# Kernel tuning notes

Hardware: AMD Instinct MI355X
Metric: run time of the kernel (lower is better)

## Reference

```python
import jax, jax.numpy as jnp
import numpy as np

B, NQ, NK = 4, 384, 384
D_EQUI, D_QINV, D_KVINV = 64, 256, 256
D_MSG, D_FF, D_OUT = 64, 128, 64
IN_FEATS = 2 * D_MSG + D_EQUI  # 192


def setup_inputs() -> dict:
    key = jax.random.key(0)
    ks = jax.random.split(key, 12)
    s = lambda k, shp, fan: jax.random.normal(k, shp, jnp.float32) / np.sqrt(fan)
    return {
        "q_equi": jax.random.normal(ks[0], (B, NQ, 3, D_EQUI), jnp.float32),
        "q_inv": jax.random.normal(ks[1], (B, NQ, D_QINV), jnp.float32),
        "k_equi": jax.random.normal(ks[2], (B, NK, 3, D_EQUI), jnp.float32),
        "k_inv": jax.random.normal(ks[3], (B, NK, D_KVINV), jnp.float32),
        "Wq": s(ks[4], (D_QINV, D_MSG), D_QINV),
        "bq": jnp.zeros((D_MSG,), jnp.float32),
        "Wk": s(ks[5], (D_KVINV, D_MSG), D_KVINV),
        "bk": jnp.zeros((D_MSG,), jnp.float32),
        "W1": s(ks[6], (IN_FEATS, D_FF), IN_FEATS),
        "b1": jnp.zeros((D_FF,), jnp.float32),
        "W2": s(ks[7], (D_FF, D_OUT), D_FF),
        "b2": jnp.zeros((D_OUT,), jnp.float32),
    }


def reference(q_equi, q_inv, k_equi, k_inv, Wq, bq, Wk, bk, W1, b1, W2, b2):
    # dotprods over the 3 spatial coords, per equi-channel: [B, Nq, Nk, d_equi]
    dotprods = jnp.einsum("bqcd,bkcd->bqkd", q_equi, k_equi)
    q_msg = q_inv @ Wq + bq  # [B, Nq, d_msg]
    k_msg = k_inv @ Wk + bk  # [B, Nk, d_msg]
    b, nq, dm = q_msg.shape
    nk = k_msg.shape[1]
    # expand + concat -> [B, Nq, Nk, in_feats]
    feats = jnp.concatenate(
        [
            jnp.broadcast_to(q_msg[:, :, None, :], (b, nq, nk, dm)),
            jnp.broadcast_to(k_msg[:, None, :, :], (b, nq, nk, dm)),
            dotprods,
        ],
        axis=-1,
    )
    h = jax.nn.silu(feats @ W1 + b1)  # [B, Nq, Nk, d_ff]
    return h @ W2 + b2  # [B, Nq, Nk, d_out]
```

## Files before the change

kernel.cpp:

```cpp
#include <hip/hip_runtime.h>
#include <stdint.h>
#include <stddef.h>

#define NQ 384
#define NK 384

typedef __attribute__((ext_vector_type(4))) float float4_;
typedef __attribute__((ext_vector_type(8))) short short8;

__device__ __forceinline__ short f2bf(float f) {
  union { float f; uint32_t u; } v; v.f = f;
  uint32_t u = v.u;
  uint32_t r = (u + 0x7fffu + ((u >> 16) & 1u)) >> 16;
  return (short)r;
}

__global__ __launch_bounds__(128) void prep_kernel(
    const float* __restrict__ q_inv, const float* __restrict__ k_inv,
    const float* __restrict__ Wq, const float* __restrict__ bq,
    const float* __restrict__ Wk, const float* __restrict__ bk,
    const float* __restrict__ W1, const float* __restrict__ b1,
    const float* __restrict__ W2,
    float* __restrict__ A1, float* __restrict__ A2,
    short* __restrict__ W1dfrag, short* __restrict__ W2frag)
{
  int bid = blockIdx.x;
  int t = threadIdx.x;

  if (bid == 3072) {
    for (int idx = t; idx < 8192; idx += 128) {
      int fi = idx >> 9;
      int l  = (idx >> 3) & 63;
      int i  = idx & 7;
      {
        int n = fi >> 1, s = fi & 1;
        int d = s * 32 + ((l >> 4) << 3) + i;
        int f = n * 16 + (l & 15);
        W1dfrag[idx] = f2bf(W1[(128 + d) * 128 + f]);
      }
      {
        int n2 = fi >> 2, s2 = fi & 3;
        int k = s2 * 32 + ((l >> 4) << 3) + i;
        int o = n2 * 16 + (l & 15);
        W2frag[idx] = f2bf(W2[k * 64 + o]);
      }
    }
    return;
  }

  int half = bid / 1536;
  int idx = bid - half * 1536;
  const float* inv  = (half ? k_inv : q_inv) + (size_t)idx * 256;
  const float* W    = half ? Wk : Wq;
  const float* bias = half ? bk : bq;

  __shared__ float sinv[256];
  __shared__ float part[2][64];
  __shared__ float smsg[64];

  sinv[t] = inv[t];
  sinv[t + 128] = inv[t + 128];
  __syncthreads();

  {
    int f = t & 63, hh = t >> 6;
    float acc = 0.f;
    const float* wp = W + hh * 128 * 64 + f;
    const float* ip = sinv + hh * 128;
    #pragma unroll 4
    for (int j = 0; j < 128; ++j) acc += ip[j] * wp[j * 64];
    part[hh][f] = acc;
  }
  __syncthreads();
  if (t < 64) smsg[t] = part[0][t] + part[1][t] + bias[t];
  __syncthreads();

  {
    int n = t;
    const float* w1p = W1 + (half ? 64 : 0) * 128 + n;
    float acc = half ? 0.f : b1[n];
    #pragma unroll 8
    for (int f = 0; f < 64; ++f) acc += smsg[f] * w1p[f * 128];
    (half ? A2 : A1)[(size_t)idx * 128 + n] = acc;
  }
}

__global__ __launch_bounds__(512) void main_kernel(
    const float* __restrict__ q_equi, const float* __restrict__ k_equi,
    const float* __restrict__ A1, const float* __restrict__ A2,
    const short* __restrict__ W1dfrag, const short* __restrict__ W2frag,
    const float* __restrict__ b2, float* __restrict__ out)
{
  int bid = blockIdx.x;
  int b = bid / 576;
  int rem = bid - b * 576;
  int tq = rem / 24, tk = rem - (rem / 24) * 24;
  int q0 = tq * 16, k0 = tk * 16;

  __shared__ __align__(16) char smem[65536];
  float* sQ = (float*)smem;
  float* sK = (float*)(smem + 13056);

  int tid = threadIdx.x;
  int w = tid >> 6, l = tid & 63;
  int g = l >> 4, r16 = l & 15;

  const float* qsrc = q_equi + ((size_t)(b * NQ + q0)) * 192;
  const float* ksrc = k_equi + ((size_t)(b * NK + k0)) * 192;
  for (int j = tid; j < 3072; j += 512) {
    int rr = j / 192, cd = j - rr * 192;
    int c = cd >> 6, d = cd & 63;
    int li = c * 1088 + rr * 68 + d;
    sQ[li] = qsrc[j];
    sK[li] = ksrc[j];
  }
  __syncthreads();

  short8 afrag[2][2];
  #pragma unroll
  for (int s = 0; s < 2; ++s) {
    int d0 = s * 32 + g * 8;
    float4_ kva[3], kvb[3];
    #pragma unroll
    for (int c = 0; c < 3; ++c) {
      kva[c] = *(const float4_*)&sK[c * 1088 + r16 * 68 + d0];
      kvb[c] = *(const float4_*)&sK[c * 1088 + r16 * 68 + d0 + 4];
    }
    #pragma unroll
    for (int m = 0; m < 2; ++m) {
      int qi = 2 * w + m;
      float4_ qva[3], qvb[3];
      #pragma unroll
      for (int c = 0; c < 3; ++c) {
        qva[c] = *(const float4_*)&sQ[c * 1088 + qi * 68 + d0];
        qvb[c] = *(const float4_*)&sQ[c * 1088 + qi * 68 + d0 + 4];
      }
      short8 af;
      #pragma unroll
      for (int i = 0; i < 4; ++i) {
        float da = qva[0][i] * kva[0][i] + qva[1][i] * kva[1][i] + qva[2][i] * kva[2][i];
        float db = qvb[0][i] * kvb[0][i] + qvb[1][i] * kvb[1][i] + qvb[2][i] * kvb[2][i];
        af[i]     = f2bf(da);
        af[i + 4] = f2bf(db);
      }
      afrag[m][s] = af;
    }
  }

  float4_ acc1[2][8];
  const float* A1p = A1 + ((size_t)(b * NQ + q0)) * 128;
  const float* A2p = A2 + ((size_t)(b * NK + k0)) * 128;
  #pragma unroll
  for (int n = 0; n < 8; ++n) {
    int f = n * 16 + r16;
    float a2v0 = A2p[(g * 4 + 0) * 128 + f];
    float a2v1 = A2p[(g * 4 + 1) * 128 + f];
    float a2v2 = A2p[(g * 4 + 2) * 128 + f];
    float a2v3 = A2p[(g * 4 + 3) * 128 + f];
    #pragma unroll
    for (int m = 0; m < 2; ++m) {
      float a1v = A1p[(2 * w + m) * 128 + f];
      acc1[m][n] = (float4_){a1v + a2v0, a1v + a2v1, a1v + a2v2, a1v + a2v3};
    }
  }
  #pragma unroll
  for (int n = 0; n < 8; ++n) {
    #pragma unroll
    for (int s = 0; s < 2; ++s) {
      short8 bf = *(const short8*)&W1dfrag[(((n * 2 + s) * 64) + l) * 8];
      #pragma unroll
      for (int m = 0; m < 2; ++m)
        acc1[m][n] = __builtin_amdgcn_mfma_f32_16x16x32_bf16(afrag[m][s], bf, acc1[m][n], 0, 0, 0);
    }
  }
  __syncthreads();

  #pragma unroll
  for (int m = 0; m < 2; ++m) {
    int pbase = (2 * w + m) * 16 + g * 4;
    #pragma unroll
    for (int n = 0; n < 8; ++n) {
      int col = n * 16 + r16;
      #pragma unroll
      for (int rr = 0; rr < 4; ++rr) {
        float x = acc1[m][n][rr];
        float sig = 1.f / (1.f + __expf(-x));
        int p = pbase + rr;
        int byte = (p * 256 + col * 2) ^ ((p & 7) << 4);
        *(short*)(smem + byte) = f2bf(x * sig);
      }
    }
  }
  __syncthreads();

  short8 w2f[4][4];
  #pragma unroll
  for (int n2 = 0; n2 < 4; ++n2)
    #pragma unroll
    for (int s2 = 0; s2 < 4; ++s2)
      w2f[n2][s2] = *(const short8*)&W2frag[(((n2 * 4 + s2) * 64) + l) * 8];

  float4_ acc2[2][4];
  #pragma unroll
  for (int m = 0; m < 2; ++m)
    #pragma unroll
    for (int n2 = 0; n2 < 4; ++n2)
      acc2[m][n2] = (float4_){0.f, 0.f, 0.f, 0.f};

  #pragma unroll
  for (int m = 0; m < 2; ++m) {
    int row = (2 * w + m) * 16 + r16;
    #pragma unroll
    for (int s2 = 0; s2 < 4; ++s2) {
      int byte = (row * 256 + (s2 * 32 + g * 8) * 2) ^ ((row & 7) << 4);
      short8 ha = *(const short8*)(smem + byte);
      #pragma unroll
      for (int n2 = 0; n2 < 4; ++n2)
        acc2[m][n2] = __builtin_amdgcn_mfma_f32_16x16x32_bf16(ha, w2f[n2][s2], acc2[m][n2], 0, 0, 0);
    }
  }

  float* outp = out + ((size_t)(b * NQ + q0) * NK + k0) * 64;
  #pragma unroll
  for (int n2 = 0; n2 < 4; ++n2) {
    float b2v = b2[n2 * 16 + r16];
    #pragma unroll
    for (int m = 0; m < 2; ++m) {
      int qi = 2 * w + m;
      #pragma unroll
      for (int rr = 0; rr < 4; ++rr) {
        int ki = g * 4 + rr;
        outp[((size_t)qi * NK + ki) * 64 + n2 * 16 + r16] = acc2[m][n2][rr] + b2v;
      }
    }
  }
}

extern "C" void kernel_launch(void* const* d_in, const int* in_sizes, int n_in,
                              void* d_out, int out_size, void* d_ws, size_t ws_size,
                              hipStream_t stream) {
  (void)in_sizes; (void)n_in; (void)out_size; (void)ws_size;
  const float* q_equi = (const float*)d_in[0];
  const float* q_inv  = (const float*)d_in[1];
  const float* k_equi = (const float*)d_in[2];
  const float* k_inv  = (const float*)d_in[3];
  const float* Wq = (const float*)d_in[4];
  const float* bq = (const float*)d_in[5];
  const float* Wk = (const float*)d_in[6];
  const float* bk = (const float*)d_in[7];
  const float* W1 = (const float*)d_in[8];
  const float* b1 = (const float*)d_in[9];
  const float* W2 = (const float*)d_in[10];
  const float* b2 = (const float*)d_in[11];
  float* out = (float*)d_out;

  char* ws = (char*)d_ws;
  float* A1      = (float*)(ws);
  float* A2      = (float*)(ws + 786432);
  short* W1dfrag = (short*)(ws + 1572864);
  short* W2frag  = (short*)(ws + 1589248);

  prep_kernel<<<3073, 128, 0, stream>>>(q_inv, k_inv, Wq, bq, Wk, bk, W1, b1, W2,
                                        A1, A2, W1dfrag, W2frag);
  main_kernel<<<2304, 512, 0, stream>>>(q_equi, k_equi, A1, A2, W1dfrag, W2frag, b2, out);
}
```

Measured before the change: 253.2 us.

## Fold projection weights into W1, transpose MFMA operands, process q rows per-wave

The prep stage now precomputes Wq·W1a and Wk·W1b plus bias constants in a small kernel, then projects q_inv/k_inv directly to 128-wide A1/A2 with 8 rows per block instead of one row per block. The main kernel swaps MFMA operand order so accumulators hold consecutive output features, allowing float4 loads of A1/A2 and float4 stores of the output. It processes each of the two q rows per wave sequentially through a per-wave LDS tile, halving shared memory and dropping a block barrier. This adds a third kernel launch and changes the fp32 association of the projection sums.

After: 295.3 us. 1.17x slower.

```diff
diff --git a/kernel.cpp b/kernel.cpp
--- a/kernel.cpp
+++ b/kernel.cpp
@@ -1,4 +1,5 @@
 #include <hip/hip_runtime.h>
+#include <hip/hip_bf16.h>
 #include <stdint.h>
 #include <stddef.h>
 
@@ -7,6 +8,7 @@
 
 typedef __attribute__((ext_vector_type(4))) float float4_;
 typedef __attribute__((ext_vector_type(8))) short short8;
+typedef __attribute__((ext_vector_type(2))) unsigned int uint2_;
 
 __device__ __forceinline__ short f2bf(float f) {
   union { float f; uint32_t u; } v; v.f = f;
@@ -15,74 +17,94 @@
   return (short)r;
 }
 
-__global__ __launch_bounds__(128) void prep_kernel(
-    const float* __restrict__ q_inv, const float* __restrict__ k_inv,
-    const float* __restrict__ Wq, const float* __restrict__ bq,
-    const float* __restrict__ Wk, const float* __restrict__ bk,
+__device__ __forceinline__ unsigned int pk2(float lo, float hi) {
+  __hip_bfloat162 r = __float22bfloat162_rn(make_float2(lo, hi));
+  union { __hip_bfloat162 b; unsigned int u; } u; u.b = r;
+  return u.u;
+}
+
+__global__ __launch_bounds__(256) void prep0(
+    const float* __restrict__ Wq, const float* __restrict__ Wk,
     const float* __restrict__ W1, const float* __restrict__ b1,
+    const float* __restrict__ bq, const float* __restrict__ bk,
     const float* __restrict__ W2,
-    float* __restrict__ A1, float* __restrict__ A2,
+    float* __restrict__ Wqc, float* __restrict__ Wkc,
+    float* __restrict__ c1, float* __restrict__ c2,
     short* __restrict__ W1dfrag, short* __restrict__ W2frag)
 {
-  int bid = blockIdx.x;
-  int t = threadIdx.x;
-
-  if (bid == 3072) {
-    for (int idx = t; idx < 8192; idx += 128) {
+  int bid = blockIdx.x, t = threadIdx.x;
+  if (bid < 32) {
+    int side = bid >> 4;
+    int r0 = (bid & 15) * 16;
+    const float* W = side ? Wk : Wq;
+    const float* W1s = W1 + side * 64 * 128;
+    float* Wc = side ? Wkc : Wqc;
+    __shared__ float sW[16][64];
+    for (int j = t; j < 1024; j += 256) sW[j >> 6][j & 63] = W[(r0 + (j >> 6)) * 64 + (j & 63)];
+    __syncthreads();
+    int c = t & 127, rg = (t >> 7) * 8;
+    float acc[8] = {0.f, 0.f, 0.f, 0.f, 0.f, 0.f, 0.f, 0.f};
+    for (int k = 0; k < 64; ++k) {
+      float wv = W1s[k * 128 + c];
+      #pragma unroll
+      for (int j = 0; j < 8; ++j) acc[j] += sW[rg + j][k] * wv;
+    }
+    for (int j = 0; j < 8; ++j) Wc[(r0 + rg + j) * 128 + c] = acc[j];
+  } else if (bid == 32) {
+    if (t < 256) {
+      int c = t & 127, side = t >> 7;
+      const float* bias = side ? bk : bq;
+      const float* W1s = W1 + side * 64 * 128;
+      float acc = side ? 0.f : b1[c];
+      for (int k = 0; k < 64; ++k) acc += bias[k] * W1s[k * 128 + c];
+      (side ? c2 : c1)[c] = acc;
+    }
+  } else {
+    for (int idx = t; idx < 8192; idx += 256) {
       int fi = idx >> 9;
       int l  = (idx >> 3) & 63;
       int i  = idx & 7;
-      {
-        int n = fi >> 1, s = fi & 1;
+      { int n = fi >> 1, s = fi & 1;
         int d = s * 32 + ((l >> 4) << 3) + i;
         int f = n * 16 + (l & 15);
-        W1dfrag[idx] = f2bf(W1[(128 + d) * 128 + f]);
-      }
-      {
-        int n2 = fi >> 2, s2 = fi & 3;
+        W1dfrag[idx] = f2bf(W1[(128 + d) * 128 + f]); }
+      { int n2 = fi >> 2, s2 = fi & 3;
         int k = s2 * 32 + ((l >> 4) << 3) + i;
         int o = n2 * 16 + (l & 15);
-        W2frag[idx] = f2bf(W2[k * 64 + o]);
-      }
-    }
-    return;
-  }
-
-  int half = bid / 1536;
-  int idx = bid - half * 1536;
-  const float* inv  = (half ? k_inv : q_inv) + (size_t)idx * 256;
-  const float* W    = half ? Wk : Wq;
-  const float* bias = half ? bk : bq;
-
-  __shared__ float sinv[256];
-  __shared__ float part[2][64];
-  __shared__ float smsg[64];
-
-  sinv[t] = inv[t];
-  sinv[t + 128] = inv[t + 128];
+        W2frag[idx] = f2bf(W2[k * 64 + o]); }
+    }
+  }
+}
+
+__global__ __launch_bounds__(256) void prep1(
+    const float* __restrict__ q_inv, const float* __restrict__ k_inv,
+    const float* __restrict__ Wqc, const float* __restrict__ Wkc,
+    const float* __restrict__ c1, const float* __restrict__ c2,
+    float* __restrict__ A1, float* __restrict__ A2)
+{
+  int bid = blockIdx.x, t = threadIdx.x;
+  int row0 = bid * 8;
+  int side = row0 >= 1536;
+  int r0 = row0 - side * 1536;
+  const float* inv = (side ? k_inv : q_inv) + (size_t)r0 * 256;
+  const float* Wc  = side ? Wkc : Wqc;
+  const float* cc  = side ? c2 : c1;
+  float* A = (side ? A2 : A1) + (size_t)r0 * 128;
+
+  __shared__ float sI[8][256];
+  for (int j = t; j < 2048; j += 256) sI[j >> 8][j & 255] = inv[j];
   __syncthreads();
 
-  {
-    int f = t & 63, hh = t >> 6;
-    float acc = 0.f;
-    const float* wp = W + hh * 128 * 64 + f;
-    const float* ip = sinv + hh * 128;
-    #pragma unroll 4
-    for (int j = 0; j < 128; ++j) acc += ip[j] * wp[j * 64];
-    part[hh][f] = acc;
-  }
-  __syncthreads();
-  if (t < 64) smsg[t] = part[0][t] + part[1][t] + bias[t];
-  __syncthreads();
-
-  {
-    int n = t;
-    const float* w1p = W1 + (half ? 64 : 0) * 128 + n;
-    float acc = half ? 0.f : b1[n];
-    #pragma unroll 8
-    for (int f = 0; f < 64; ++f) acc += smsg[f] * w1p[f * 128];
-    (half ? A2 : A1)[(size_t)idx * 128 + n] = acc;
-  }
+  int c = t & 127, rg = (t >> 7) * 4;
+  float acc[4] = {0.f, 0.f, 0.f, 0.f};
+  for (int k = 0; k < 256; ++k) {
+    float wv = Wc[k * 128 + c];
+    #pragma unroll
+    for (int j = 0; j < 4; ++j) acc[j] += sI[rg + j][k] * wv;
+  }
+  float cv = cc[c];
+  #pragma unroll
+  for (int j = 0; j < 4; ++j) A[(size_t)(rg + j) * 128 + c] = acc[j] + cv;
 }
 
 __global__ __launch_bounds__(512) void main_kernel(
@@ -97,7 +119,7 @@
   int tq = rem / 24, tk = rem - (rem / 24) * 24;
   int q0 = tq * 16, k0 = tk * 16;
 
-  __shared__ __align__(16) char smem[65536];
+  __shared__ __align__(16) char smem[32768];
   float* sQ = (float*)smem;
   float* sK = (float*)(smem + 13056);
 
@@ -135,103 +157,85 @@
         qva[c] = *(const float4_*)&sQ[c * 1088 + qi * 68 + d0];
         qvb[c] = *(const float4_*)&sQ[c * 1088 + qi * 68 + d0 + 4];
       }
-      short8 af;
+      float da[4], db[4];
       #pragma unroll
       for (int i = 0; i < 4; ++i) {
-        float da = qva[0][i] * kva[0][i] + qva[1][i] * kva[1][i] + qva[2][i] * kva[2][i];
-        float db = qvb[0][i] * kvb[0][i] + qvb[1][i] * kvb[1][i] + qvb[2][i] * kvb[2][i];
-        af[i]     = f2bf(da);
-        af[i + 4] = f2bf(db);
-      }
-      afrag[m][s] = af;
-    }
-  }
-
-  float4_ acc1[2][8];
+        da[i] = qva[0][i] * kva[0][i] + qva[1][i] * kva[1][i] + qva[2][i] * kva[2][i];
+        db[i] = qvb[0][i] * kvb[0][i] + qvb[1][i] * kvb[1][i] + qvb[2][i] * kvb[2][i];
+      }
+      union { short8 s8; unsigned int u[4]; } au;
+      au.u[0] = pk2(da[0], da[1]);
+      au.u[1] = pk2(da[2], da[3]);
+      au.u[2] = pk2(db[0], db[1]);
+      au.u[3] = pk2(db[2], db[3]);
+      afrag[m][s] = au.s8;
+    }
+  }
+  __syncthreads();
+
+  char* hbase = smem + w * 4096;
   const float* A1p = A1 + ((size_t)(b * NQ + q0)) * 128;
   const float* A2p = A2 + ((size_t)(b * NK + k0)) * 128;
-  #pragma unroll
-  for (int n = 0; n < 8; ++n) {
-    int f = n * 16 + r16;
-    float a2v0 = A2p[(g * 4 + 0) * 128 + f];
-    float a2v1 = A2p[(g * 4 + 1) * 128 + f];
-    float a2v2 = A2p[(g * 4 + 2) * 128 + f];
-    float a2v3 = A2p[(g * 4 + 3) * 128 + f];
-    #pragma unroll
-    for (int m = 0; m < 2; ++m) {
-      float a1v = A1p[(2 * w + m) * 128 + f];
-      acc1[m][n] = (float4_){a1v + a2v0, a1v + a2v1, a1v + a2v2, a1v + a2v3};
-    }
-  }
-  #pragma unroll
-  for (int n = 0; n < 8; ++n) {
-    #pragma unroll
-    for (int s = 0; s < 2; ++s) {
-      short8 bf = *(const short8*)&W1dfrag[(((n * 2 + s) * 64) + l) * 8];
-      #pragma unroll
-      for (int m = 0; m < 2; ++m)
-        acc1[m][n] = __builtin_amdgcn_mfma_f32_16x16x32_bf16(afrag[m][s], bf, acc1[m][n], 0, 0, 0);
-    }
-  }
-  __syncthreads();
+
+  float4_ b2v[4];
+  #pragma unroll
+  for (int ot = 0; ot < 4; ++ot)
+    b2v[ot] = *(const float4_*)&b2[ot * 16 + g * 4];
 
   #pragma unroll
   for (int m = 0; m < 2; ++m) {
-    int pbase = (2 * w + m) * 16 + g * 4;
-    #pragma unroll
-    for (int n = 0; n < 8; ++n) {
-      int col = n * 16 + r16;
-      #pragma unroll
-      for (int rr = 0; rr < 4; ++rr) {
-        float x = acc1[m][n][rr];
-        float sig = 1.f / (1.f + __expf(-x));
-        int p = pbase + rr;
-        int byte = (p * 256 + col * 2) ^ ((p & 7) << 4);
-        *(short*)(smem + byte) = f2bf(x * sig);
-      }
-    }
-  }
-  __syncthreads();
-
-  short8 w2f[4][4];
-  #pragma unroll
-  for (int n2 = 0; n2 < 4; ++n2)
-    #pragma unroll
-    for (int s2 = 0; s2 < 4; ++s2)
-      w2f[n2][s2] = *(const short8*)&W2frag[(((n2 * 4 + s2) * 64) + l) * 8];
-
-  float4_ acc2[2][4];
-  #pragma unroll
-  for (int m = 0; m < 2; ++m)
-    #pragma unroll
-    for (int n2 = 0; n2 < 4; ++n2)
-      acc2[m][n2] = (float4_){0.f, 0.f, 0.f, 0.f};
-
-  #pragma unroll
-  for (int m = 0; m < 2; ++m) {
-    int row = (2 * w + m) * 16 + r16;
+    int qi = 2 * w + m;
+
+    float4_ acc1[8];
+    #pragma unroll
+    for (int ft = 0; ft < 8; ++ft) {
+      float4_ a1v = *(const float4_*)&A1p[qi * 128 + ft * 16 + g * 4];
+      float4_ a2v = *(const float4_*)&A2p[r16 * 128 + ft * 16 + g * 4];
+      acc1[ft] = a1v + a2v;
+    }
+
+    #pragma unroll
+    for (int ft = 0; ft < 8; ++ft) {
+      #pragma unroll
+      for (int s = 0; s < 2; ++s) {
+        short8 wf = *(const short8*)&W1dfrag[(((ft * 2 + s) * 64) + l) * 8];
+        acc1[ft] = __builtin_amdgcn_mfma_f32_16x16x32_bf16(wf, afrag[m][s], acc1[ft], 0, 0, 0);
+      }
+    }
+
+    #pragma unroll
+    for (int ft = 0; ft < 8; ++ft) {
+      float4_ x = acc1[ft];
+      float y0 = x[0] / (1.f + __expf(-x[0]));
+      float y1 = x[1] / (1.f + __expf(-x[1]));
+      float y2 = x[2] / (1.f + __expf(-x[2]));
+      float y3 = x[3] / (1.f + __expf(-x[3]));
+      uint2_ pv;
+      pv[0] = pk2(y0, y1);
+      pv[1] = pk2(y2, y3);
+      int byte = (r16 * 256 + ft * 32 + g * 8) ^ ((r16 & 7) << 4);
+      *(uint2_*)(hbase + byte) = pv;
+    }
+
+    float4_ acc2[4];
+    #pragma unroll
+    for (int ot = 0; ot < 4; ++ot) acc2[ot] = (float4_){0.f, 0.f, 0.f, 0.f};
     #pragma unroll
     for (int s2 = 0; s2 < 4; ++s2) {
-      int byte = (row * 256 + (s2 * 32 + g * 8) * 2) ^ ((row & 7) << 4);
-      short8 ha = *(const short8*)(smem + byte);
-      #pragma unroll
-      for (int n2 = 0; n2 < 4; ++n2)
-        acc2[m][n2] = __builtin_amdgcn_mfma_f32_16x16x32_bf16(ha, w2f[n2][s2], acc2[m][n2], 0, 0, 0);
-    }
-  }
-
-  float* outp = out + ((size_t)(b * NQ + q0) * NK + k0) * 64;
-  #pragma unroll
-  for (int n2 = 0; n2 < 4; ++n2) {
-    float b2v = b2[n2 * 16 + r16];
-    #pragma unroll
-    for (int m = 0; m < 2; ++m) {
-      int qi = 2 * w + m;
-      #pragma unroll
-      for (int rr = 0; rr < 4; ++rr) {
-        int ki = g * 4 + rr;
-        outp[((size_t)qi * NK + ki) * 64 + n2 * 16 + r16] = acc2[m][n2][rr] + b2v;
-      }
+      int byte = (r16 * 256 + s2 * 64 + g * 16) ^ ((r16 & 7) << 4);
+      short8 hb = *(const short8*)(hbase + byte);
+      #pragma unroll
+      for (int ot = 0; ot < 4; ++ot) {
+        short8 wf = *(const short8*)&W2frag[(((ot * 4 + s2) * 64) + l) * 8];
+        acc2[ot] = __builtin_amdgcn_mfma_f32_16x16x32_bf16(wf, hb, acc2[ot], 0, 0, 0);
+      }
+    }
+
+    float* op = out + ((size_t)(b * NQ + q0 + qi) * NK + k0 + r16) * 64;
+    #pragma unroll
+    for (int ot = 0; ot < 4; ++ot) {
+      float4_ o4 = acc2[ot] + b2v[ot];
+      *(float4_*)(op + ot * 16 + g * 4) = o4;
     }
   }
 }
@@ -259,8 +263,12 @@
   float* A2      = (float*)(ws + 786432);
   short* W1dfrag = (short*)(ws + 1572864);
   short* W2frag  = (short*)(ws + 1589248);
-
-  prep_kernel<<<3073, 128, 0, stream>>>(q_inv, k_inv, Wq, bq, Wk, bk, W1, b1, W2,
-                                        A1, A2, W1dfrag, W2frag);
+  float* Wqc     = (float*)(ws + 1605632);
+  float* Wkc     = (float*)(ws + 1736704);
+  float* c1      = (float*)(ws + 1867776);
+  float* c2      = (float*)(ws + 1868288);
+
+  prep0<<<34, 256, 0, stream>>>(Wq, Wk, W1, b1, bq, bk, W2, Wqc, Wkc, c1, c2, W1dfrag, W2frag);
+  prep1<<<384, 256, 0, stream>>>(q_inv, k_inv, Wqc, Wkc, c1, c2, A1, A2);
   main_kernel<<<2304, 512, 0, stream>>>(q_equi, k_equi, A1, A2, W1dfrag, W2frag, b2, out);
 }
```
